# Kernel optimization log

Measured on AMD Instinct MI355X. Metric: run time of the kernel, lower is better.

## Reference

```python
import jax, jax.numpy as jnp
import numpy as np

B, S, H, I, E, K = 4, 2048, 2048, 5632, 8, 2


def setup_inputs() -> dict:
    key = jax.random.key(0)
    k0, k1, k2, k3, k4 = jax.random.split(key, 5)
    std_p = 1.0 / np.sqrt(H)
    return {
        "hidden_states": jax.random.normal(k0, (B, S, H), dtype=jnp.float32),
        "router_w": jax.random.normal(k1, (E, H), dtype=jnp.float32) * 0.02,
        "w_gate": jax.random.normal(k2, (E, H, I), dtype=jnp.float32) * std_p,
        "w_up": jax.random.normal(k3, (E, H, I), dtype=jnp.float32) * std_p,
        "w_down": jax.random.normal(k4, (E, I, H), dtype=jnp.float32) * (1.0 / np.sqrt(I)),
    }


def reference(hidden_states, router_w, w_gate, w_up, w_down):
    b, s, h = hidden_states.shape
    x = hidden_states.reshape(-1, h)                       # [T, H]
    router_logits = x @ router_w.T                          # [T, E]
    routing_weights = jax.nn.softmax(router_logits, axis=-1)
    top_w, top_i = jax.lax.top_k(routing_weights, K)        # [T, K]
    top_w = top_w / jnp.sum(top_w, axis=-1, keepdims=True)  # renormalize over top-k
    # combine[t, e] = sum_k top_w[t, k] * (top_i[t, k] == e)
    combine = jnp.sum(jax.nn.one_hot(top_i, E, dtype=top_w.dtype) * top_w[..., None], axis=1)  # [T, E]
    out = jnp.zeros_like(x)
    for e in range(E):  # small fixed expert count
        # SwiGLU expert MLP: down(silu(gate(x)) * up(x))
        act = jax.nn.silu(x @ w_gate[e]) * (x @ w_up[e])    # [T, I]
        out = out + (act @ w_down[e]) * combine[:, e:e + 1]
    return (out.reshape(b, s, h),
            router_logits.reshape(b, s, E),
            top_i.reshape(b, s, K),
            top_w.reshape(b, s, K))
```

## Files before the change

### kernel.cpp

```cpp
#include <hip/hip_runtime.h>
#include <hip/hip_bf16.h>
#include <stdint.h>

#define NTOK 8192
#define HD   2048
#define ID   5632
#define NE   8
#define NASSIGN (NTOK * 2)
#define MAXT256 (NASSIGN / 256 + NE)

typedef __attribute__((ext_vector_type(8))) short  bf16x8;
typedef __attribute__((ext_vector_type(4))) float  f32x4;
typedef __attribute__((ext_vector_type(8))) unsigned short u16x8;

__device__ __forceinline__ unsigned short f2bf(float f) {
  union { float f; unsigned int u; } c; c.f = f;
  unsigned int lsb = (c.u >> 16) & 1u;
  return (unsigned short)((c.u + 0x7fffu + lsb) >> 16);
}
__device__ __forceinline__ float bf2f(unsigned short u) {
  union { float f; unsigned int u; } c; c.u = ((unsigned int)u) << 16;
  return c.f;
}

__device__ __forceinline__ void async16(const void* g, void* l) {
  __builtin_amdgcn_global_load_lds(
      (const __attribute__((address_space(1))) void*)g,
      (__attribute__((address_space(3))) void*)l, 16, 0, 0);
}

__global__ __launch_bounds__(256) void k_router(
    const float* __restrict__ x, const float* __restrict__ rw,
    float* __restrict__ out_logits, float* __restrict__ out_topi,
    float* __restrict__ out_topw,
    int* __restrict__ tk_e, float* __restrict__ tk_w, int* __restrict__ cnts)
{
  const int wid = threadIdx.x >> 6, lane = threadIdx.x & 63;
  const int t = blockIdx.x * 4 + wid;
  const float* xr = x + (size_t)t * HD;
  float acc[NE];
#pragma unroll
  for (int e = 0; e < NE; e++) acc[e] = 0.f;
#pragma unroll
  for (int i = 0; i < 8; i++) {
    const int col = lane * 4 + i * 256;
    const float4 xv = *(const float4*)(xr + col);
#pragma unroll
    for (int e = 0; e < NE; e++) {
      const float4 wv = *(const float4*)(rw + e * HD + col);
      acc[e] += xv.x * wv.x + xv.y * wv.y + xv.z * wv.z + xv.w * wv.w;
    }
  }
#pragma unroll
  for (int e = 0; e < NE; e++)
    for (int o = 32; o >= 1; o >>= 1) acc[e] += __shfl_xor(acc[e], o, 64);

  if (lane == 0) {
    int i1 = 0;
#pragma unroll
    for (int e = 1; e < NE; e++) if (acc[e] > acc[i1]) i1 = e;
    int i2 = (i1 == 0) ? 1 : 0;
#pragma unroll
    for (int e = 0; e < NE; e++) if (e != i1 && acc[e] > acc[i2]) i2 = e;
    float p2 = __expf(acc[i2] - acc[i1]);
    float s  = 1.f + p2;
    float w1 = 1.f / s, w2 = p2 / s;
#pragma unroll
    for (int e = 0; e < NE; e++) out_logits[(size_t)t * NE + e] = acc[e];
    out_topi[t * 2 + 0] = (float)i1; out_topi[t * 2 + 1] = (float)i2;
    out_topw[t * 2 + 0] = w1;        out_topw[t * 2 + 1] = w2;
    tk_e[t * 2 + 0] = i1; tk_e[t * 2 + 1] = i2;
    tk_w[t * 2 + 0] = w1; tk_w[t * 2 + 1] = w2;
    atomicAdd(&cnts[i1], 1); atomicAdd(&cnts[i2], 1);
  }
}

__global__ void k_scan(const int* __restrict__ cnts, int* __restrict__ offs,
                       int* __restrict__ cursor, int* __restrict__ tile_e,
                       int* __restrict__ tile_rt, int* __restrict__ ntiles) {
  if (threadIdx.x == 0) {
    int s = 0, nt = 0;
    for (int e = 0; e < NE; e++) {
      offs[e] = s; cursor[e] = s;
      int ntl = (cnts[e] + 255) >> 8;
      for (int i = 0; i < ntl; i++) { tile_e[nt] = e; tile_rt[nt] = i; nt++; }
      s += cnts[e];
    }
    ntiles[0] = nt;
  }
}

__global__ void k_assign(const int* __restrict__ tk_e, const float* __restrict__ tk_w,
                         int* __restrict__ cursor, int* __restrict__ perm,
                         float* __restrict__ pw, int* __restrict__ inv) {
  int t = blockIdx.x * 256 + threadIdx.x;
  if (t >= NTOK) return;
#pragma unroll
  for (int k = 0; k < 2; k++) {
    int e = tk_e[t * 2 + k];
    int pos = atomicAdd(&cursor[e], 1);
    perm[pos] = t;
    pw[pos] = tk_w[t * 2 + k];
    inv[t * 2 + k] = pos;
  }
}

__global__ __launch_bounds__(256) void k_gather(const float* __restrict__ x,
    const int* __restrict__ perm, unsigned short* __restrict__ xg) {
  const int r = blockIdx.x;
  const int tok = perm[r];
  const float* src = x + (size_t)tok * HD;
  unsigned short* dst = xg + (size_t)r * HD;
  const int c = threadIdx.x * 8;
  float4 a = *(const float4*)(src + c);
  float4 b = *(const float4*)(src + c + 4);
  u16x8 o;
  o[0] = f2bf(a.x); o[1] = f2bf(a.y); o[2] = f2bf(a.z); o[3] = f2bf(a.w);
  o[4] = f2bf(b.x); o[5] = f2bf(b.y); o[6] = f2bf(b.z); o[7] = f2bf(b.w);
  *(u16x8*)(dst + c) = o;
}

__global__ __launch_bounds__(256) void k_conv_gu(const float* __restrict__ wg,
    const float* __restrict__ wu, unsigned short* __restrict__ wgT,
    unsigned short* __restrict__ wuT) {
  __shared__ float tl[32][33];
  const int z = blockIdx.z, e = z >> 1;
  const float* in = ((z & 1) ? wu : wg) + (size_t)e * HD * ID;
  unsigned short* out = ((z & 1) ? wuT : wgT) + (size_t)e * (size_t)ID * HD;
  const int tx = threadIdx.x & 31, ty = threadIdx.x >> 5;
  const int c0 = blockIdx.x * 32, r0 = blockIdx.y * 32;
#pragma unroll
  for (int j = 0; j < 4; j++)
    tl[ty + j * 8][tx] = in[(size_t)(r0 + ty + j * 8) * ID + (c0 + tx)];
  __syncthreads();
#pragma unroll
  for (int j = 0; j < 4; j++) {
    int oc = ty + j * 8;
    out[(size_t)(c0 + oc) * HD + (r0 + tx)] = f2bf(tl[tx][oc]);
  }
}

__global__ __launch_bounds__(256) void k_conv_d(const float* __restrict__ wd,
    unsigned short* __restrict__ wdT) {
  __shared__ float tl[32][33];
  const int e = blockIdx.z;
  const float* in = wd + (size_t)e * ID * HD;
  unsigned short* out = wdT + (size_t)e * (size_t)HD * ID;
  const int tx = threadIdx.x & 31, ty = threadIdx.x >> 5;
  const int c0 = blockIdx.x * 32, r0 = blockIdx.y * 32;
#pragma unroll
  for (int j = 0; j < 4; j++)
    tl[ty + j * 8][tx] = in[(size_t)(r0 + ty + j * 8) * HD + (c0 + tx)];
  __syncthreads();
#pragma unroll
  for (int j = 0; j < 4; j++) {
    int oc = ty + j * 8;
    out[(size_t)(c0 + oc) * ID + (r0 + tx)] = f2bf(tl[tx][oc]);
  }
}

#define HB(b,kh,op) (((((b)*2+(kh))*2)+(op))*16384)

template <int EPI, int NMAT, int KMAT>
__global__ __launch_bounds__(512, 2) void k_gemm256(
    const unsigned short* __restrict__ A, const unsigned short* __restrict__ Wbase,
    const int* __restrict__ cnts, const int* __restrict__ offs,
    const int* __restrict__ tile_e, const int* __restrict__ tile_rt,
    const int* __restrict__ ntiles,
    unsigned short* __restrict__ gtmp, unsigned short* __restrict__ gact,
    const float* __restrict__ pw, float* __restrict__ dbuf)
{
  const int raw = blockIdx.x;
  const int v = (raw & 7) * ((int)gridDim.x >> 3) + (raw >> 3);
  const int ct = v / MAXT256;
  const int ti = v % MAXT256;
  if (ti >= ntiles[0]) return;
  const int e = tile_e[ti], rt = tile_rt[ti];
  const int cnt = cnts[e], off = offs[e];
  const int tid = threadIdx.x;

  __shared__ __align__(16) char smem[131072];

  const unsigned short* W = Wbase + (size_t)e * (size_t)NMAT * KMAT;
  const size_t arow0 = (size_t)off + (size_t)rt * 256;
  const size_t bcol0 = (size_t)ct * 256;

  const int u0 = tid, u1 = 512 + tid;
  const int r0s = ((u0 >> 3) << 1) | (((u0 >> 2) & 1) ^ ((u0 >> 4) & 1));
  const int c0s = ((u0 & 3) ^ (r0s & 3)) * 8;
  const int r1s = ((u1 >> 3) << 1) | (((u1 >> 2) & 1) ^ ((u1 >> 4) & 1));
  const int c1s = ((u1 & 3) ^ (r1s & 3)) * 8;

  const int NT = KMAT / 64, NIT = NT / 2;

  auto STAGE_A = [&](int bb, int kh, int kt) {
    const int kc = kt * 64 + kh * 32;
    async16(A + (arow0 + r0s) * (size_t)KMAT + kc + c0s, smem + HB(bb,kh,0) + tid * 16);
    async16(A + (arow0 + r1s) * (size_t)KMAT + kc + c1s, smem + HB(bb,kh,0) + 8192 + tid * 16);
  };
  auto STAGE_B = [&](int bb, int kh, int kt) {
    const int kc = kt * 64 + kh * 32;
    async16(W + (bcol0 + r0s) * (size_t)KMAT + kc + c0s, smem + HB(bb,kh,1) + tid * 16);
    async16(W + (bcol0 + r1s) * (size_t)KMAT + kc + c1s, smem + HB(bb,kh,1) + 8192 + tid * 16);
  };

  f32x4 acc[8][4];
#pragma unroll
  for (int m = 0; m < 8; m++)
#pragma unroll
    for (int n = 0; n < 4; n++) acc[m][n] = (f32x4)0.f;

  const int lane = tid & 63, wid = tid >> 6;
  const int wm = wid >> 2, wn = wid & 3;
  const int fr = lane & 15;
  const int slotp = (lane >> 4) ^ (fr & 3);
  const int laddr = ((fr << 6) | (slotp << 4)) ^ ((fr & 4) << 4);

  STAGE_A(0,0,0); STAGE_B(0,0,0); STAGE_A(0,1,0); STAGE_B(0,1,0);
  STAGE_A(1,0,1); STAGE_B(1,0,1);
  asm volatile("s_waitcnt vmcnt(4)");
  asm volatile("s_barrier" ::: "memory");

  constexpr int SB[8]  = {1,1,0,0,0,0,1,1};
  constexpr int SOP[8] = {0,1,0,1,0,1,0,1};
  constexpr int SKH[8] = {1,1,0,0,1,1,0,0};
  constexpr int SKO[8] = {1,1,2,2,2,2,3,3};

  bf16x8 bfr[4];
  for (int i = 0; i < NIT; ++i) {
#pragma unroll
    for (int p = 0; p < 8; ++p) {
      const int b = p >> 2, kh = (p >> 1) & 1, mh = p & 1;
      bf16x8 afr[4];
#pragma unroll
      for (int t = 0; t < 4; t++)
        afr[t] = *(const bf16x8*)(smem + HB(b,kh,0) + ((wm*128 + mh*64 + t*16) << 6) + laddr);
      if (mh == 0) {
#pragma unroll
        for (int t = 0; t < 4; t++)
          bfr[t] = *(const bf16x8*)(smem + HB(b,kh,1) + ((wn*64 + t*16) << 6) + laddr);
      }
      {
        int kt = 2 * i + SKO[p]; kt = kt < NT - 1 ? kt : NT - 1;
        if (SOP[p] == 0) STAGE_A(SB[p], SKH[p], kt);
        else             STAGE_B(SB[p], SKH[p], kt);
      }
      asm volatile("s_barrier" ::: "memory");
      __builtin_amdgcn_s_setprio(1);
#pragma unroll
      for (int t = 0; t < 4; t++)
#pragma unroll
        for (int n = 0; n < 4; n++)
          acc[mh*4 + t][n] = __builtin_amdgcn_mfma_f32_16x16x32_bf16(afr[t], bfr[n], acc[mh*4 + t][n], 0, 0, 0);
      __builtin_amdgcn_s_setprio(0);
      if (p == 3 || p == 7) asm volatile("s_waitcnt vmcnt(4)");
      asm volatile("s_barrier" ::: "memory");
    }
  }
  asm volatile("s_waitcnt vmcnt(0)");

  const int crow = (lane >> 4) * 4, ccol = lane & 15;
  const int rbase = rt * 256 + wm * 128;
#pragma unroll
  for (int mt = 0; mt < 8; ++mt) {
#pragma unroll
    for (int j = 0; j < 4; ++j) {
      const int rl = rbase + mt * 16 + crow + j;
      if (rl >= cnt) continue;
      const size_t grow = (size_t)off + rl;
      float wgt = 0.f;
      if (EPI == 2) wgt = pw[grow];
#pragma unroll
      for (int nt = 0; nt < 4; ++nt) {
        const int col = (int)bcol0 + wn * 64 + nt * 16 + ccol;
        const float vv = acc[mt][nt][j];
        if (EPI == 0) {
          gtmp[grow * (size_t)NMAT + col] = f2bf(vv);
        } else if (EPI == 1) {
          const float g = bf2f(gtmp[grow * (size_t)NMAT + col]);
          const float a = g / (1.f + __expf(-g)) * vv;
          gact[grow * (size_t)NMAT + col] = f2bf(a);
        } else {
          dbuf[grow * (size_t)NMAT + col] = vv * wgt;
        }
      }
    }
  }
}

__global__ __launch_bounds__(256) void k_combine(const float* __restrict__ dbuf,
    const int* __restrict__ inv, float* __restrict__ out) {
  const int t = blockIdx.x;
  const int p0 = inv[t * 2], p1 = inv[t * 2 + 1];
  const float4* r0 = (const float4*)(dbuf + (size_t)p0 * HD);
  const float4* r1 = (const float4*)(dbuf + (size_t)p1 * HD);
  float4* o = (float4*)(out + (size_t)t * HD);
#pragma unroll
  for (int i = 0; i < 2; i++) {
    int c = threadIdx.x + i * 256;
    float4 a = r0[c], b = r1[c];
    o[c] = make_float4(a.x + b.x, a.y + b.y, a.z + b.z, a.w + b.w);
  }
}

extern "C" void kernel_launch(void* const* d_in, const int* in_sizes, int n_in,
                              void* d_out, int out_size, void* d_ws, size_t ws_size,
                              hipStream_t stream) {
  const float* x  = (const float*)d_in[0];
  const float* rw = (const float*)d_in[1];
  const float* wg = (const float*)d_in[2];
  const float* wu = (const float*)d_in[3];
  const float* wd = (const float*)d_in[4];

  float* outp       = (float*)d_out;
  float* out_logits = outp + (size_t)NTOK * HD;
  float* out_topi   = out_logits + (size_t)NTOK * NE;
  float* out_topw   = out_topi + (size_t)NTOK * 2;

  char* w = (char*)d_ws;
  int*   cnts    = (int*)(w + 0);
  int*   offs    = (int*)(w + 64);
  int*   cursor  = (int*)(w + 128);
  int*   ntiles  = (int*)(w + 192);
  int*   tile_e  = (int*)(w + 256);
  int*   tile_rt = (int*)(w + 1280);
  int*   tk_e    = (int*)(w + 4096);
  float* tk_w    = (float*)(w + 4096 + 65536);
  int*   perm    = (int*)(w + 4096 + 2 * 65536);
  float* pw      = (float*)(w + 4096 + 3 * 65536);
  int*   inv     = (int*)(w + 4096 + 4 * 65536);

  char* big = w + (1 << 20);
  unsigned short* xg = (unsigned short*)big;
  const size_t XG_E = (size_t)(NASSIGN + 256) * HD;
  unsigned short* wgT = xg + XG_E;
  const size_t WT_E = (size_t)NE * ID * HD;
  unsigned short* wuT  = wgT + WT_E;
  unsigned short* wdT  = wuT + WT_E;
  unsigned short* gtmp = wdT + WT_E;
  const size_t GA_E = (size_t)(NASSIGN + 256) * ID;
  unsigned short* gact = gtmp + GA_E;
  float* dbuf = (float*)(gact + GA_E);

  hipMemsetAsync(d_ws, 0, 256, stream);

  k_conv_gu<<<dim3(ID / 32, HD / 32, 2 * NE), 256, 0, stream>>>(wg, wu, wgT, wuT);
  k_conv_d<<<dim3(HD / 32, ID / 32, NE), 256, 0, stream>>>(wd, wdT);

  k_router<<<NTOK / 4, 256, 0, stream>>>(x, rw, out_logits, out_topi, out_topw,
                                         tk_e, tk_w, cnts);
  k_scan<<<1, 64, 0, stream>>>(cnts, offs, cursor, tile_e, tile_rt, ntiles);
  k_assign<<<NTOK / 256, 256, 0, stream>>>(tk_e, tk_w, cursor, perm, pw, inv);
  k_gather<<<NASSIGN, 256, 0, stream>>>(x, perm, xg);

  k_gemm256<0, ID, HD><<<dim3((ID / 256) * MAXT256), 512, 0, stream>>>(
      xg, wgT, cnts, offs, tile_e, tile_rt, ntiles, gtmp, nullptr, nullptr, nullptr);
  k_gemm256<1, ID, HD><<<dim3((ID / 256) * MAXT256), 512, 0, stream>>>(
      xg, wuT, cnts, offs, tile_e, tile_rt, ntiles, gtmp, gact, nullptr, nullptr);
  k_gemm256<2, HD, ID><<<dim3((HD / 256) * MAXT256), 512, 0, stream>>>(
      gact, wdT, cnts, offs, tile_e, tile_rt, ntiles, nullptr, nullptr, pw, dbuf);

  k_combine<<<NTOK, 256, 0, stream>>>(dbuf, inv, outp);
}
```

Before: 2.053 ms.

## Double-buffer LDS fragment loads to prefetch next phase during MFMA

The MoE GEMM inner loop now keeps current and next register fragment sets, loading the next phase's A/B fragments from shared memory before issuing the current phase's MFMAs. The vmcnt wait is moved earlier and loosened to vmcnt(2), and memory clobbers are added to the waits. This is meant to hide LDS read latency behind matrix math. In exchange it uses more VGPRs, which can lower occupancy, and the changed wait placement risks reading staged data before it is ready.

New measurement: 2.067 ms. No clear change (+0.7%).

```diff
diff --git a/kernel.cpp b/kernel.cpp
--- a/kernel.cpp
+++ b/kernel.cpp
@@ -218,7 +218,7 @@
 
   STAGE_A(0,0,0); STAGE_B(0,0,0); STAGE_A(0,1,0); STAGE_B(0,1,0);
   STAGE_A(1,0,1); STAGE_B(1,0,1);
-  asm volatile("s_waitcnt vmcnt(4)");
+  asm volatile("s_waitcnt vmcnt(4)" ::: "memory");
   asm volatile("s_barrier" ::: "memory");
 
   constexpr int SB[8]  = {1,1,0,0,0,0,1,1};
@@ -226,19 +226,26 @@
   constexpr int SKH[8] = {1,1,0,0,1,1,0,0};
   constexpr int SKO[8] = {1,1,2,2,2,2,3,3};
 
-  bf16x8 bfr[4];
+  bf16x8 afr_c[4], bfr_c[4], afr_n[4], bfr_n[4];
+#pragma unroll
+  for (int t = 0; t < 4; t++) {
+    afr_c[t] = *(const bf16x8*)(smem + HB(0,0,0) + ((wm*128 + t*16) << 6) + laddr);
+    bfr_c[t] = *(const bf16x8*)(smem + HB(0,0,1) + ((wn*64 + t*16) << 6) + laddr);
+  }
+
   for (int i = 0; i < NIT; ++i) {
 #pragma unroll
     for (int p = 0; p < 8; ++p) {
-      const int b = p >> 2, kh = (p >> 1) & 1, mh = p & 1;
-      bf16x8 afr[4];
+      const int np = (p + 1) & 7;
+      const int nb = np >> 2, nkh = (np >> 1) & 1, nmh = np & 1;
+      if (p == 3 || p == 7) asm volatile("s_waitcnt vmcnt(2)" ::: "memory");
 #pragma unroll
       for (int t = 0; t < 4; t++)
-        afr[t] = *(const bf16x8*)(smem + HB(b,kh,0) + ((wm*128 + mh*64 + t*16) << 6) + laddr);
-      if (mh == 0) {
+        afr_n[t] = *(const bf16x8*)(smem + HB(nb,nkh,0) + ((wm*128 + nmh*64 + t*16) << 6) + laddr);
+      if (p & 1) {
 #pragma unroll
         for (int t = 0; t < 4; t++)
-          bfr[t] = *(const bf16x8*)(smem + HB(b,kh,1) + ((wn*64 + t*16) << 6) + laddr);
+          bfr_n[t] = *(const bf16x8*)(smem + HB(nb,nkh,1) + ((wn*64 + t*16) << 6) + laddr);
       }
       {
         int kt = 2 * i + SKO[p]; kt = kt < NT - 1 ? kt : NT - 1;
@@ -247,17 +254,25 @@
       }
       asm volatile("s_barrier" ::: "memory");
       __builtin_amdgcn_s_setprio(1);
-#pragma unroll
-      for (int t = 0; t < 4; t++)
-#pragma unroll
-        for (int n = 0; n < 4; n++)
-          acc[mh*4 + t][n] = __builtin_amdgcn_mfma_f32_16x16x32_bf16(afr[t], bfr[n], acc[mh*4 + t][n], 0, 0, 0);
+      {
+        const int mh = p & 1;
+#pragma unroll
+        for (int t = 0; t < 4; t++)
+#pragma unroll
+          for (int n = 0; n < 4; n++)
+            acc[mh*4 + t][n] = __builtin_amdgcn_mfma_f32_16x16x32_bf16(afr_c[t], bfr_c[n], acc[mh*4 + t][n], 0, 0, 0);
+      }
       __builtin_amdgcn_s_setprio(0);
-      if (p == 3 || p == 7) asm volatile("s_waitcnt vmcnt(4)");
       asm volatile("s_barrier" ::: "memory");
+#pragma unroll
+      for (int t = 0; t < 4; t++) afr_c[t] = afr_n[t];
+      if (p & 1) {
+#pragma unroll
+        for (int t = 0; t < 4; t++) bfr_c[t] = bfr_n[t];
+      }
     }
   }
-  asm volatile("s_waitcnt vmcnt(0)");
+  asm volatile("s_waitcnt vmcnt(0)" ::: "memory");
 
   const int crow = (lane >> 4) * 4, ccol = lane & 15;
   const int rbase = rt * 256 + wm * 128;
```

## Remap GEMM block order per XCD for tile locality and simplify LDS swizzle

Applied to the files above, without the earlier changes.

Changes how block indices map to (column tile, row tile) so each XCD owns a contiguous slice of row tiles, with blocks grouped in pairs or triples of row tiles that sweep all column tiles. The goal is better L2 reuse of A and weight tiles within each XCD. It also replaces the LDS staging and read swizzle with a simpler row/slot XOR pattern and adds memory clobbers to the waitcnt asm. The new swizzle may change LDS bank conflicts. The mapping assumes MAXT256 divides evenly by 8 and that chunk counts line up; otherwise some tiles could be skipped or duplicated.

New measurement: 2.097 ms. +2.2%, slower.

```diff
diff --git a/kernel.cpp b/kernel.cpp
--- a/kernel.cpp
+++ b/kernel.cpp
@@ -8,6 +8,7 @@
 #define NE   8
 #define NASSIGN (NTOK * 2)
 #define MAXT256 (NASSIGN / 256 + NE)
+#define TPX (MAXT256 / 8)
 
 typedef __attribute__((ext_vector_type(8))) short  bf16x8;
 typedef __attribute__((ext_vector_type(4))) float  f32x4;
@@ -161,7 +162,7 @@
 
 #define HB(b,kh,op) (((((b)*2+(kh))*2)+(op))*16384)
 
-template <int EPI, int NMAT, int KMAT>
+template <int EPI, int NMAT, int KMAT, int NCT, int PAIR>
 __global__ __launch_bounds__(512, 2) void k_gemm256(
     const unsigned short* __restrict__ A, const unsigned short* __restrict__ Wbase,
     const int* __restrict__ cnts, const int* __restrict__ offs,
@@ -171,9 +172,12 @@
     const float* __restrict__ pw, float* __restrict__ dbuf)
 {
   const int raw = blockIdx.x;
-  const int v = (raw & 7) * ((int)gridDim.x >> 3) + (raw >> 3);
-  const int ct = v / MAXT256;
-  const int ti = v % MAXT256;
+  const int xcd = raw & 7;
+  const int v   = raw >> 3;
+  const int chunk = v / (NCT * PAIR);
+  const int r     = v % (NCT * PAIR);
+  const int ct   = r / PAIR;
+  const int ti   = xcd * TPX + chunk * PAIR + (r % PAIR);
   if (ti >= ntiles[0]) return;
   const int e = tile_e[ti], rt = tile_rt[ti];
   const int cnt = cnts[e], off = offs[e];
@@ -185,11 +189,10 @@
   const size_t arow0 = (size_t)off + (size_t)rt * 256;
   const size_t bcol0 = (size_t)ct * 256;
 
-  const int u0 = tid, u1 = 512 + tid;
-  const int r0s = ((u0 >> 3) << 1) | (((u0 >> 2) & 1) ^ ((u0 >> 4) & 1));
-  const int c0s = ((u0 & 3) ^ (r0s & 3)) * 8;
-  const int r1s = ((u1 >> 3) << 1) | (((u1 >> 2) & 1) ^ ((u1 >> 4) & 1));
-  const int c1s = ((u1 & 3) ^ (r1s & 3)) * 8;
+  const int r0s = tid >> 2;
+  const int c0s = (((tid & 3) ^ ((tid >> 3) & 3)) * 8);
+  const int r1s = 128 + (tid >> 2);
+  const int c1s = c0s;
 
   const int NT = KMAT / 64, NIT = NT / 2;
 
@@ -213,12 +216,12 @@
   const int lane = tid & 63, wid = tid >> 6;
   const int wm = wid >> 2, wn = wid & 3;
   const int fr = lane & 15;
-  const int slotp = (lane >> 4) ^ (fr & 3);
-  const int laddr = ((fr << 6) | (slotp << 4)) ^ ((fr & 4) << 4);
+  const int slot = ((lane >> 4) ^ ((fr >> 1) & 3));
+  const int laddr = (fr << 6) + (slot << 4);
 
   STAGE_A(0,0,0); STAGE_B(0,0,0); STAGE_A(0,1,0); STAGE_B(0,1,0);
   STAGE_A(1,0,1); STAGE_B(1,0,1);
-  asm volatile("s_waitcnt vmcnt(4)");
+  asm volatile("s_waitcnt vmcnt(4)" ::: "memory");
   asm volatile("s_barrier" ::: "memory");
 
   constexpr int SB[8]  = {1,1,0,0,0,0,1,1};
@@ -253,11 +256,11 @@
         for (int n = 0; n < 4; n++)
           acc[mh*4 + t][n] = __builtin_amdgcn_mfma_f32_16x16x32_bf16(afr[t], bfr[n], acc[mh*4 + t][n], 0, 0, 0);
       __builtin_amdgcn_s_setprio(0);
-      if (p == 3 || p == 7) asm volatile("s_waitcnt vmcnt(4)");
+      if (p == 3 || p == 7) asm volatile("s_waitcnt vmcnt(4)" ::: "memory");
       asm volatile("s_barrier" ::: "memory");
     }
   }
-  asm volatile("s_waitcnt vmcnt(0)");
+  asm volatile("s_waitcnt vmcnt(0)" ::: "memory");
 
   const int crow = (lane >> 4) * 4, ccol = lane & 15;
   const int rbase = rt * 256 + wm * 128;
@@ -353,11 +356,11 @@
   k_assign<<<NTOK / 256, 256, 0, stream>>>(tk_e, tk_w, cursor, perm, pw, inv);
   k_gather<<<NASSIGN, 256, 0, stream>>>(x, perm, xg);
 
-  k_gemm256<0, ID, HD><<<dim3((ID / 256) * MAXT256), 512, 0, stream>>>(
+  k_gemm256<0, ID, HD, 22, 3><<<dim3(22 * MAXT256), 512, 0, stream>>>(
       xg, wgT, cnts, offs, tile_e, tile_rt, ntiles, gtmp, nullptr, nullptr, nullptr);
-  k_gemm256<1, ID, HD><<<dim3((ID / 256) * MAXT256), 512, 0, stream>>>(
+  k_gemm256<1, ID, HD, 22, 3><<<dim3(22 * MAXT256), 512, 0, stream>>>(
       xg, wuT, cnts, offs, tile_e, tile_rt, ntiles, gtmp, gact, nullptr, nullptr);
-  k_gemm256<2, HD, ID><<<dim3((HD / 256) * MAXT256), 512, 0, stream>>>(
+  k_gemm256<2, HD, ID, 8, 1><<<dim3(8 * MAXT256), 512, 0, stream>>>(
       gact, wdT, cnts, offs, tile_e, tile_rt, ntiles, nullptr, nullptr, pw, dbuf);
 
   k_combine<<<NTOK, 256, 0, stream>>>(dbuf, inv, outp);
```
